# Kernel optimization log

Hardware: AMD Instinct MI355X
Metric: run time of the kernel (lower is better)

The kernel has to match this reference:

```python
import jax, jax.numpy as jnp
import numpy as np

HIDDEN = 24
INPUT_DIM = 2
T = 262
K_INFO = 256
BATCH = 8192


def _gru_scan(gi_tm, h0, w_hh, b_hh):
    """Run a GRU over time-major precomputed input gates.

    gi_tm: (T, B, 3H) = x @ W_ih^T + b_ih, already in time order to process.
    Returns (T, B, H) hidden states.
    PyTorch gate order: [r, z, n].
    """
    H = HIDDEN

    def step(h, gi):
        gh = h @ w_hh.T + b_hh  # (B, 3H)
        r = jax.nn.sigmoid(gi[:, :H] + gh[:, :H])
        z = jax.nn.sigmoid(gi[:, H:2 * H] + gh[:, H:2 * H])
        n = jnp.tanh(gi[:, 2 * H:] + r * gh[:, 2 * H:])
        h_new = (1.0 - z) * n + z * h
        return h_new, h_new

    _, hs = jax.lax.scan(step, h0, gi_tm)
    return hs  # (T, B, H)


def setup_inputs() -> dict:
    key = jax.random.key(0)
    ks = jax.random.split(key, 11)
    s = 1.0 / np.sqrt(HIDDEN)  # torch RNN init scale
    u = lambda k, shape: jax.random.uniform(k, shape, jnp.float32, -s, s)
    return {
        "x": jax.random.normal(ks[0], (BATCH, T, INPUT_DIM), jnp.float32),
        "w_ih_f": u(ks[1], (3 * HIDDEN, INPUT_DIM)),
        "w_hh_f": u(ks[2], (3 * HIDDEN, HIDDEN)),
        "b_ih_f": u(ks[3], (3 * HIDDEN,)),
        "b_hh_f": u(ks[4], (3 * HIDDEN,)),
        "w_ih_b": u(ks[5], (3 * HIDDEN, INPUT_DIM)),
        "w_hh_b": u(ks[6], (3 * HIDDEN, HIDDEN)),
        "b_ih_b": u(ks[7], (3 * HIDDEN,)),
        "b_hh_b": u(ks[8], (3 * HIDDEN,)),
        "w_out": u(ks[9], (1, 2 * HIDDEN)),
        "b_out": u(ks[10], (1,)),
    }


def reference(x, w_ih_f, w_hh_f, b_ih_f, b_hh_f,
              w_ih_b, w_hh_b, b_ih_b, b_hh_b, w_out, b_out):
    B = x.shape[0]
    h0 = jnp.zeros((B, HIDDEN), x.dtype)
    x_tm = jnp.transpose(x, (1, 0, 2))  # (T, B, D) time-major

    # Precompute input-gate projections for whole sequence (one big GEMM each).
    gi_f = jnp.einsum('tbd,gd->tbg', x_tm, w_ih_f) + b_ih_f  # (T, B, 3H)
    gi_b = jnp.einsum('tbd,gd->tbg', x_tm, w_ih_b) + b_ih_b

    hs_f = _gru_scan(gi_f, h0, w_hh_f, b_hh_f)                  # (T, B, H)
    hs_b = _gru_scan(gi_b[::-1], h0, w_hh_b, b_hh_b)[::-1]      # reverse dir

    rnn_out = jnp.concatenate([hs_f, hs_b], axis=-1)            # (T, B, 2H)
    rnn_out = jnp.transpose(rnn_out, (1, 0, 2))                 # (B, T, 2H)

    logits = jnp.einsum('btg,og->bto', rnn_out, w_out)[..., 0] + b_out[0]
    return logits[:, :K_INFO]  # (B, 256)
```

## Files before the change

### kernel.cpp

```cpp
#include <hip/hip_runtime.h>

#define HID  24
#define TT   262
#define KOUT 256
#define BPB  8
#define PSTR 260

typedef _Float16 h2 __attribute__((ext_vector_type(2)));

#define DOT2(acc, a, b) asm("v_dot2_f32_f16 %0, %1, %2, %0" : "+v"(acc) : "v"(a), "v"(b))
#define OPAQUE(x)       asm volatile("" : "+v"(x))

__device__ __forceinline__ float sig2(float x){
    return __builtin_amdgcn_rcpf(1.0f + __builtin_amdgcn_exp2f(x));
}
__device__ __forceinline__ h2 pk(float a, float b){
    h2 r; r.x = (_Float16)a; r.y = (_Float16)b; return r;
}

__device__ __forceinline__ float dpp_sum32(float v){
    int x;
    x = __builtin_amdgcn_update_dpp(0, __builtin_bit_cast(int, v), 0x111, 0xf, 0xf, true); v += __builtin_bit_cast(float, x);
    x = __builtin_amdgcn_update_dpp(0, __builtin_bit_cast(int, v), 0x112, 0xf, 0xf, true); v += __builtin_bit_cast(float, x);
    x = __builtin_amdgcn_update_dpp(0, __builtin_bit_cast(int, v), 0x114, 0xf, 0xf, true); v += __builtin_bit_cast(float, x);
    x = __builtin_amdgcn_update_dpp(0, __builtin_bit_cast(int, v), 0x118, 0xf, 0xf, true); v += __builtin_bit_cast(float, x);
    x = __builtin_amdgcn_update_dpp(0, __builtin_bit_cast(int, v), 0x142, 0xf, 0xf, true); v += __builtin_bit_cast(float, x);
    return v;
}

template<bool FWD>
__device__ __forceinline__ void run_dir(
    const float* xrow,
    uint* hrow,
    float* prow,
    const float* __restrict__ w_ih, const float* __restrict__ w_hh,
    const float* __restrict__ b_ih, const float* __restrict__ b_hh,
    const float* __restrict__ w_out, int lane)
{
    const int   ii  = (lane < HID) ? lane : 0;
    const float msk = (lane < HID) ? 1.0f : 0.0f;

    const float SRZ = -1.4426950408889634f * msk;
    const float SN  =  2.8853900817779268f * msk;

    const float4* r4 = reinterpret_cast<const float4*>(w_hh + ii * HID);
    const float4* z4 = reinterpret_cast<const float4*>(w_hh + (HID + ii) * HID);
    const float4* n4 = reinterpret_cast<const float4*>(w_hh + (2 * HID + ii) * HID);

    h2 wr0,wr1,wr2,wr3,wr4,wr5,wr6,wr7,wr8,wr9,wr10,wr11;
    h2 wz0,wz1,wz2,wz3,wz4,wz5,wz6,wz7,wz8,wz9,wz10,wz11;
    h2 wn0,wn1,wn2,wn3,wn4,wn5,wn6,wn7,wn8,wn9,wn10,wn11;
#define LDW(d0, d1, Q, S) { float4 q_ = (Q); d0 = pk(q_.x*(S), q_.y*(S)); d1 = pk(q_.z*(S), q_.w*(S)); OPAQUE(d0); OPAQUE(d1); }
    LDW(wr0, wr1, r4[0], SRZ) LDW(wr2, wr3, r4[1], SRZ) LDW(wr4, wr5, r4[2], SRZ)
    LDW(wr6, wr7, r4[3], SRZ) LDW(wr8, wr9, r4[4], SRZ) LDW(wr10,wr11,r4[5], SRZ)
    LDW(wz0, wz1, z4[0], SRZ) LDW(wz2, wz3, z4[1], SRZ) LDW(wz4, wz5, z4[2], SRZ)
    LDW(wz6, wz7, z4[3], SRZ) LDW(wz8, wz9, z4[4], SRZ) LDW(wz10,wz11,z4[5], SRZ)
    LDW(wn0, wn1, n4[0], SN ) LDW(wn2, wn3, n4[1], SN ) LDW(wn4, wn5, n4[2], SN )
    LDW(wn6, wn7, n4[3], SN ) LDW(wn8, wn9, n4[4], SN ) LDW(wn10,wn11,n4[5], SN )
#undef LDW

    h2 wxr = pk(w_ih[2*ii] * SRZ,          w_ih[2*ii+1] * SRZ);
    h2 wxz = pk(w_ih[2*(HID+ii)] * SRZ,    w_ih[2*(HID+ii)+1] * SRZ);
    h2 wxn = pk(w_ih[2*(2*HID+ii)] * SN,   w_ih[2*(2*HID+ii)+1] * SN);
    float br  = (b_ih[ii]       + b_hh[ii])       * SRZ;
    float bz  = (b_ih[HID+ii]   + b_hh[HID+ii])   * SRZ;
    float bnh =  b_hh[2*HID+ii] * SN;
    float bni =  b_ih[2*HID+ii] * SN;
    float pw  =  w_out[(FWD ? 0 : HID) + ii] * msk;
    OPAQUE(wxr); OPAQUE(wxz); OPAQUE(wxn);

    float hself = 0.0f;
    reinterpret_cast<_Float16*>(hrow)[lane] = (_Float16)0.0f;
    asm volatile("" ::: "memory");

    const uint4* h16 = reinterpret_cast<const uint4*>(hrow);
    int t = FWD ? 0 : (TT - 1);
    const int steps = FWD ? KOUT : TT;

    #pragma unroll 1
    for (int s = 0; s < steps; ++s){
        const float2 xv = *reinterpret_cast<const float2*>(xrow + 2 * t);
        const h2 xp = __builtin_bit_cast(h2, __builtin_amdgcn_cvt_pkrtz(xv.x, xv.y));

        float ar = br, az = bz, an = bnh, ai = bni;
        uint4 q; h2 hp;
#define D3(u, WR, WZ, WN) { hp = __builtin_bit_cast(h2, (u)); DOT2(ar, hp, WR); DOT2(az, hp, WZ); DOT2(an, hp, WN); }
        q = h16[0];
        D3(q.x, wr0, wz0, wn0) D3(q.y, wr1, wz1, wn1) D3(q.z, wr2, wz2, wn2) D3(q.w, wr3, wz3, wn3)
        q = h16[1];
        D3(q.x, wr4, wz4, wn4) D3(q.y, wr5, wz5, wn5) D3(q.z, wr6, wz6, wn6) D3(q.w, wr7, wz7, wn7)
        q = h16[2];
        D3(q.x, wr8, wz8, wn8) D3(q.y, wr9, wz9, wn9) D3(q.z, wr10,wz10,wn10) D3(q.w, wr11,wz11,wn11)
#undef D3
        DOT2(ar, xp, wxr);
        DOT2(az, xp, wxz);
        DOT2(ai, xp, wxn);

        float r = sig2(ar);
        float z = sig2(az);
        float Y = fmaf(r, an, ai);
        float n = fmaf(-2.0f, __builtin_amdgcn_rcpf(1.0f + __builtin_amdgcn_exp2f(Y)), 1.0f);
        float hnew = fmaf(z, hself - n, n);
        hself = hnew;
        reinterpret_cast<_Float16*>(hrow)[lane] = (_Float16)hnew;

        float pv = dpp_sum32(hnew * pw);
        if (FWD){
            if (lane == 31) prow[t] = pv;
        } else {
            if (lane == 31 && t < KOUT) prow[t] += pv;
        }
        asm volatile("" ::: "memory");
        t += FWD ? 1 : -1;
    }
}

__global__
__attribute__((amdgpu_flat_work_group_size(256, 256)))
__attribute__((amdgpu_waves_per_eu(4, 4)))
void birnn_kernel(
    const float* __restrict__ x,
    const float* __restrict__ w_ih_f, const float* __restrict__ w_hh_f,
    const float* __restrict__ b_ih_f, const float* __restrict__ b_hh_f,
    const float* __restrict__ w_ih_b, const float* __restrict__ w_hh_b,
    const float* __restrict__ b_ih_b, const float* __restrict__ b_hh_b,
    const float* __restrict__ w_out,  const float* __restrict__ b_out,
    float* __restrict__ out)
{
    __shared__ __align__(16) float4 xs4[BPB * TT * 2 / 4];
    __shared__ __align__(16) uint   hsm[BPB][16];
    __shared__ float  psm[BPB][PSTR];

    const int tid  = threadIdx.x;
    const int g    = tid >> 5;
    const int lane = tid & 31;
    const int b0   = blockIdx.x * BPB;

    const float4* xg = reinterpret_cast<const float4*>(x + (size_t)b0 * (TT * 2));
    for (int i = tid; i < BPB * TT * 2 / 4; i += 256) xs4[i] = xg[i];
    __syncthreads();

    const float* xrow = reinterpret_cast<const float*>(xs4) + g * (TT * 2);
    run_dir<true >(xrow, hsm[g], psm[g], w_ih_f, w_hh_f, b_ih_f, b_hh_f, w_out, lane);
    run_dir<false>(xrow, hsm[g], psm[g], w_ih_b, w_hh_b, b_ih_b, b_hh_b, w_out, lane);
    __syncthreads();

    const float bo = b_out[0];
    for (int i = tid; i < BPB * KOUT; i += 256){
        int bl = i >> 8, t = i & 255;
        out[(size_t)(b0 + bl) * KOUT + t] = psm[bl][t] + bo;
    }
}

extern "C" void kernel_launch(void* const* d_in, const int* in_sizes, int n_in,
                              void* d_out, int out_size, void* d_ws, size_t ws_size,
                              hipStream_t stream)
{
    const float* x      = (const float*)d_in[0];
    const float* w_ih_f = (const float*)d_in[1];
    const float* w_hh_f = (const float*)d_in[2];
    const float* b_ih_f = (const float*)d_in[3];
    const float* b_hh_f = (const float*)d_in[4];
    const float* w_ih_b = (const float*)d_in[5];
    const float* w_hh_b = (const float*)d_in[6];
    const float* b_ih_b = (const float*)d_in[7];
    const float* b_hh_b = (const float*)d_in[8];
    const float* w_out  = (const float*)d_in[9];
    const float* b_out  = (const float*)d_in[10];
    float* out = (float*)d_out;

    birnn_kernel<<<dim3(8192 / BPB), dim3(256), 0, stream>>>(
        x, w_ih_f, w_hh_f, b_ih_f, b_hh_f,
        w_ih_b, w_hh_b, b_ih_b, b_hh_b, w_out, b_out, out);
}
```

Measured before the change: 395.7 us.

## Run forward and backward GRU directions concurrently in the two wave halves

Restructures the kernel so each 64-thread block handles one batch element: lanes 0-31 run the forward recurrence and lanes 32-63 the backward recurrence simultaneously, instead of one half-wave running both directions back to back. This roughly halves the serial step chain per wave. The two partial projections are summed from separate shared buffers at the end. The forward half now does 262 steps instead of 256, and a higher waves-per-EU target may pressure registers.

```diff
diff --git a/kernel.cpp b/kernel.cpp
--- a/kernel.cpp
+++ b/kernel.cpp
@@ -3,8 +3,6 @@
 #define HID  24
 #define TT   262
 #define KOUT 256
-#define BPB  8
-#define PSTR 260
 
 typedef _Float16 h2 __attribute__((ext_vector_type(2)));
 
@@ -28,17 +26,39 @@
     return v;
 }
 
-template<bool FWD>
-__device__ __forceinline__ void run_dir(
-    const float* xrow,
-    uint* hrow,
-    float* prow,
-    const float* __restrict__ w_ih, const float* __restrict__ w_hh,
-    const float* __restrict__ b_ih, const float* __restrict__ b_hh,
-    const float* __restrict__ w_out, int lane)
+__global__ __launch_bounds__(64)
+__attribute__((amdgpu_waves_per_eu(8)))
+void birnn_kernel(
+    const float* __restrict__ x,
+    const float* __restrict__ w_ih_f, const float* __restrict__ w_hh_f,
+    const float* __restrict__ b_ih_f, const float* __restrict__ b_hh_f,
+    const float* __restrict__ w_ih_b, const float* __restrict__ w_hh_b,
+    const float* __restrict__ b_ih_b, const float* __restrict__ b_hh_b,
+    const float* __restrict__ w_out,  const float* __restrict__ b_out,
+    float* __restrict__ out)
 {
-    const int   ii  = (lane < HID) ? lane : 0;
-    const float msk = (lane < HID) ? 1.0f : 0.0f;
+    __shared__ __align__(16) float4 xs4[(TT * 2) / 4];
+    __shared__ __align__(16) uint   hh[32];
+    __shared__ float psf[KOUT];
+    __shared__ float psb[KOUT];
+
+    const int tid  = threadIdx.x;
+    const int half = tid >> 5;
+    const int ul   = tid & 31;
+    const int e    = blockIdx.x;
+
+    const float4* xg = reinterpret_cast<const float4*>(x + (size_t)e * (TT * 2));
+    for (int i = tid; i < (TT * 2) / 4; i += 64) xs4[i] = xg[i];
+    __syncthreads();
+    const float* xlds = reinterpret_cast<const float*>(xs4);
+
+    const float* w_ih = half ? w_ih_b : w_ih_f;
+    const float* w_hh = half ? w_hh_b : w_hh_f;
+    const float* b_ih = half ? b_ih_b : b_ih_f;
+    const float* b_hh = half ? b_hh_b : b_hh_f;
+
+    const int   ii  = (ul < HID) ? ul : 0;
+    const float msk = (ul < HID) ? 1.0f : 0.0f;
 
     const float SRZ = -1.4426950408889634f * msk;
     const float SN  =  2.8853900817779268f * msk;
@@ -66,20 +86,21 @@
     float bz  = (b_ih[HID+ii]   + b_hh[HID+ii])   * SRZ;
     float bnh =  b_hh[2*HID+ii] * SN;
     float bni =  b_ih[2*HID+ii] * SN;
-    float pw  =  w_out[(FWD ? 0 : HID) + ii] * msk;
+    float pw  =  w_out[(half ? HID : 0) + ii] * msk;
     OPAQUE(wxr); OPAQUE(wxz); OPAQUE(wxn);
 
+    float* pdst = half ? psb : psf;
+
     float hself = 0.0f;
-    reinterpret_cast<_Float16*>(hrow)[lane] = (_Float16)0.0f;
+    reinterpret_cast<_Float16*>(hh)[tid] = (_Float16)0.0f;
     asm volatile("" ::: "memory");
 
-    const uint4* h16 = reinterpret_cast<const uint4*>(hrow);
-    int t = FWD ? 0 : (TT - 1);
-    const int steps = FWD ? KOUT : TT;
+    const uint4* h16 = reinterpret_cast<const uint4*>(hh) + (half << 2);
 
     #pragma unroll 1
-    for (int s = 0; s < steps; ++s){
-        const float2 xv = *reinterpret_cast<const float2*>(xrow + 2 * t);
+    for (int s = 0; s < TT; ++s){
+        const int tcur = half ? (TT - 1 - s) : s;
+        const float2 xv = *reinterpret_cast<const float2*>(xlds + 2 * tcur);
         const h2 xp = __builtin_bit_cast(h2, __builtin_amdgcn_cvt_pkrtz(xv.x, xv.y));
 
         float ar = br, az = bz, an = bnh, ai = bni;
@@ -102,54 +123,17 @@
         float n = fmaf(-2.0f, __builtin_amdgcn_rcpf(1.0f + __builtin_amdgcn_exp2f(Y)), 1.0f);
         float hnew = fmaf(z, hself - n, n);
         hself = hnew;
-        reinterpret_cast<_Float16*>(hrow)[lane] = (_Float16)hnew;
+        reinterpret_cast<_Float16*>(hh)[tid] = (_Float16)hnew;
 
         float pv = dpp_sum32(hnew * pw);
-        if (FWD){
-            if (lane == 31) prow[t] = pv;
-        } else {
-            if (lane == 31 && t < KOUT) prow[t] += pv;
-        }
+        if (ul == 31 && tcur < KOUT) pdst[tcur] = pv;
         asm volatile("" ::: "memory");
-        t += FWD ? 1 : -1;
     }
-}
-
-__global__
-__attribute__((amdgpu_flat_work_group_size(256, 256)))
-__attribute__((amdgpu_waves_per_eu(4, 4)))
-void birnn_kernel(
-    const float* __restrict__ x,
-    const float* __restrict__ w_ih_f, const float* __restrict__ w_hh_f,
-    const float* __restrict__ b_ih_f, const float* __restrict__ b_hh_f,
-    const float* __restrict__ w_ih_b, const float* __restrict__ w_hh_b,
-    const float* __restrict__ b_ih_b, const float* __restrict__ b_hh_b,
-    const float* __restrict__ w_out,  const float* __restrict__ b_out,
-    float* __restrict__ out)
-{
-    __shared__ __align__(16) float4 xs4[BPB * TT * 2 / 4];
-    __shared__ __align__(16) uint   hsm[BPB][16];
-    __shared__ float  psm[BPB][PSTR];
-
-    const int tid  = threadIdx.x;
-    const int g    = tid >> 5;
-    const int lane = tid & 31;
-    const int b0   = blockIdx.x * BPB;
-
-    const float4* xg = reinterpret_cast<const float4*>(x + (size_t)b0 * (TT * 2));
-    for (int i = tid; i < BPB * TT * 2 / 4; i += 256) xs4[i] = xg[i];
-    __syncthreads();
-
-    const float* xrow = reinterpret_cast<const float*>(xs4) + g * (TT * 2);
-    run_dir<true >(xrow, hsm[g], psm[g], w_ih_f, w_hh_f, b_ih_f, b_hh_f, w_out, lane);
-    run_dir<false>(xrow, hsm[g], psm[g], w_ih_b, w_hh_b, b_ih_b, b_hh_b, w_out, lane);
     __syncthreads();
 
     const float bo = b_out[0];
-    for (int i = tid; i < BPB * KOUT; i += 256){
-        int bl = i >> 8, t = i & 255;
-        out[(size_t)(b0 + bl) * KOUT + t] = psm[bl][t] + bo;
-    }
+    for (int k = tid; k < KOUT; k += 64)
+        out[(size_t)e * KOUT + k] = psf[k] + psb[k] + bo;
 }
 
 extern "C" void kernel_launch(void* const* d_in, const int* in_sizes, int n_in,
@@ -169,7 +153,7 @@
     const float* b_out  = (const float*)d_in[10];
     float* out = (float*)d_out;
 
-    birnn_kernel<<<dim3(8192 / BPB), dim3(256), 0, stream>>>(
+    birnn_kernel<<<dim3(8192), dim3(64), 0, stream>>>(
         x, w_ih_f, w_hh_f, b_ih_f, b_hh_f,
         w_ih_b, w_hh_b, b_ih_b, b_hh_b, w_out, b_out, out);
 }
```

Result: no change. 394.5 us (-0.3%).
